# Performance work log

Measured on AMD Instinct MI355X. Metric: run time of the kernel, lower is better.

Reference implementation:

```python
import jax, jax.numpy as jnp
import numpy as np

D_MODEL = 1024
N_HEADS = 16
HEAD_DIM = D_MODEL // N_HEADS


def setup_inputs() -> dict:
    key = jax.random.key(0)
    ks = jax.random.split(key, 5)
    s_in = 1.0 / np.sqrt(D_MODEL)
    x = jax.random.normal(ks[0], (4, 2048, D_MODEL), dtype=jnp.float32)
    w_qkv = jax.random.uniform(ks[1], (3 * D_MODEL, D_MODEL), dtype=jnp.float32, minval=-s_in, maxval=s_in)
    b_qkv = jax.random.uniform(ks[2], (3 * D_MODEL,), dtype=jnp.float32, minval=-s_in, maxval=s_in)
    w_out = jax.random.uniform(ks[3], (D_MODEL, D_MODEL), dtype=jnp.float32, minval=-s_in, maxval=s_in)
    b_out = jax.random.uniform(ks[4], (D_MODEL,), dtype=jnp.float32, minval=-s_in, maxval=s_in)
    return {"x": x, "w_qkv": w_qkv, "b_qkv": b_qkv, "w_out": w_out, "b_out": b_out}


def reference(x, w_qkv, b_qkv, w_out, b_out):
    B, T, D = x.shape
    H, hd = N_HEADS, HEAD_DIM
    qkv = x @ w_qkv.T + b_qkv                      # [B, T, 3D]
    q, k, v = jnp.split(qkv, 3, axis=-1)
    # [B, H, T, hd]
    q = q.reshape(B, T, H, hd).transpose(0, 2, 1, 3)
    k = k.reshape(B, T, H, hd).transpose(0, 2, 1, 3)
    v = v.reshape(B, T, H, hd).transpose(0, 2, 1, 3)
    scale = 1.0 / np.sqrt(hd).astype(np.float32)
    attn = jnp.einsum('bhqd,bhkd->bhqk', q, k) * scale
    causal = jnp.triu(jnp.ones((T, T), dtype=bool), k=1)
    attn = jnp.where(causal, -jnp.inf, attn)
    attn = jax.nn.softmax(attn, axis=-1)
    out = jnp.einsum('bhqk,bhkd->bhqd', attn, v)
    out = out.transpose(0, 2, 1, 3).reshape(B, T, D)
    return out @ w_out.T + b_out
```

## Files before the change

### kernel.cpp

```cpp
#include <hip/hip_runtime.h>
#include <hip/hip_bf16.h>
#include <stdint.h>

#define D_MODEL 1024
#define NHEADS 16
#define HD 64
#define BB 4
#define TT 2048
#define MM (BB*TT)
#define NQKV (3*D_MODEL)
#define KK D_MODEL

typedef __attribute__((ext_vector_type(4))) float f32x4;
typedef __attribute__((ext_vector_type(8))) short bf16x8;

__device__ __forceinline__ unsigned short f2bf(float x){
    union { __hip_bfloat16 h; unsigned short u; } c;
    c.h = __float2bfloat16(x);
    return c.u;
}

__device__ __forceinline__ void gload_lds16(const void* g, void* l){
    __builtin_amdgcn_global_load_lds(
        (const __attribute__((address_space(1))) unsigned int*)g,
        (__attribute__((address_space(3))) unsigned int*)l,
        16, 0, 0);
}

__global__ void cast_kernel(const float* __restrict__ in,
                            unsigned short* __restrict__ out, int n4){
    int i = blockIdx.x * blockDim.x + threadIdx.x;
    if (i >= n4) return;
    float4 v = reinterpret_cast<const float4*>(in)[i];
    ushort4 o;
    o.x = f2bf(v.x); o.y = f2bf(v.y); o.z = f2bf(v.z); o.w = f2bf(v.w);
    reinterpret_cast<ushort4*>(out)[i] = o;
}

__global__ __launch_bounds__(256) void gemm_qkv(
    const unsigned short* __restrict__ A, const unsigned short* __restrict__ Bw,
    const float* __restrict__ bias,
    unsigned short* __restrict__ qb, unsigned short* __restrict__ kb,
    unsigned short* __restrict__ vtb)
{
    __shared__ alignas(16) unsigned short As[128*32];
    __shared__ alignas(16) unsigned short Bs[128*32];
    const int tiles_n = NQKV/128;
    int bm = (blockIdx.x / tiles_n) * 128;
    int bn = (blockIdx.x % tiles_n) * 128;
    int tid = threadIdx.x;
    int w = tid >> 6, l = tid & 63;
    int wr = (w >> 1) * 64, wc = (w & 1) * 64;
    int lr = l & 15, hi = l >> 4;

    f32x4 acc[4][4] = {};

    int srow = tid >> 2;
    int scol = (tid & 3) * 8;
    const unsigned short* Ap = A + (size_t)(bm + srow) * KK + scol;
    const unsigned short* Bp = Bw + (size_t)(bn + srow) * KK + scol;
    char* AsB = (char*)As + w * 1024;
    char* BsB = (char*)Bs + w * 1024;

    for (int k0 = 0; k0 < KK; k0 += 32) {
        __syncthreads();
        gload_lds16(Ap + k0,           AsB);
        gload_lds16(Ap + 64*KK + k0,   AsB + 4096);
        gload_lds16(Bp + k0,           BsB);
        gload_lds16(Bp + 64*KK + k0,   BsB + 4096);
        __syncthreads();
        bf16x8 af[4], bfr[4];
        #pragma unroll
        for (int m = 0; m < 4; m++)
            af[m] = *reinterpret_cast<const bf16x8*>(&As[(wr + m*16 + lr)*32 + hi*8]);
        #pragma unroll
        for (int n = 0; n < 4; n++)
            bfr[n] = *reinterpret_cast<const bf16x8*>(&Bs[(wc + n*16 + lr)*32 + hi*8]);
        #pragma unroll
        for (int m = 0; m < 4; m++)
            #pragma unroll
            for (int n = 0; n < 4; n++)
                acc[m][n] = __builtin_amdgcn_mfma_f32_16x16x32_bf16(af[m], bfr[n], acc[m][n], 0, 0, 0);
    }

    #pragma unroll
    for (int m = 0; m < 4; m++) {
        int gm = bm + wr + m*16 + hi*4;
        int b  = gm >> 11;
        int t  = gm & 2047;
        #pragma unroll
        for (int n = 0; n < 4; n++) {
            int gn = bn + wc + n*16 + lr;
            float bv = bias[gn];
            int sec = gn >> 10;
            int nn  = gn & 1023;
            int h = nn >> 6, d = nn & 63;
            int bh = b * NHEADS + h;
            if (sec == 2) {
                ushort4 pk;
                pk.x = f2bf(acc[m][n][0] + bv);
                pk.y = f2bf(acc[m][n][1] + bv);
                pk.z = f2bf(acc[m][n][2] + bv);
                pk.w = f2bf(acc[m][n][3] + bv);
                *reinterpret_cast<ushort4*>(&vtb[((size_t)bh*HD + d)*TT + t]) = pk;
            } else {
                unsigned short* dst = (sec == 0) ? qb : kb;
                #pragma unroll
                for (int r = 0; r < 4; r++)
                    dst[((size_t)bh*TT + t + r)*HD + d] = f2bf(acc[m][n][r] + bv);
            }
        }
    }
}

__global__ __launch_bounds__(512) void attn_kernel(
    const unsigned short* __restrict__ qb, const unsigned short* __restrict__ kb,
    const unsigned short* __restrict__ vtb, unsigned short* __restrict__ ao)
{
    __shared__ alignas(16) unsigned short Kb[2][64*64];
    __shared__ alignas(16) unsigned short Vb[2][64*64];
    __shared__ alignas(16) unsigned short Pl[8][16*64];

    const int bh = blockIdx.x;
    const int qt = (gridDim.y - 1) - blockIdx.y;
    const int tid = threadIdx.x;
    const int w = tid >> 6, l = tid & 63;
    const int lr = l & 15, hi = l >> 4;

    const int qbase = qt * 128;
    const int qrow  = qbase + w*16;
    const int ktmax = 2*qt + 1;

    const unsigned short* Qp = qb + ((size_t)bh*TT + qrow) * HD;
    bf16x8 qf0 = *reinterpret_cast<const bf16x8*>(Qp + lr*HD + hi*8);
    bf16x8 qf1 = *reinterpret_cast<const bf16x8*>(Qp + lr*HD + 32 + hi*8);

    const unsigned short* Kg = kb  + (size_t)bh*TT*HD;
    const unsigned short* Vg = vtb + (size_t)bh*HD*TT;

    const int srow = w*8 + (l >> 3);
    const int sc16 = (l & 7) ^ (srow & 7);
    char* KbL[2] = { (char*)&Kb[0][0] + w*1024, (char*)&Kb[1][0] + w*1024 };
    char* VbL[2] = { (char*)&Vb[0][0] + w*1024, (char*)&Vb[1][0] + w*1024 };

    gload_lds16(Kg + (size_t)srow*HD + sc16*8, KbL[0]);
    gload_lds16(Vg + (size_t)srow*TT + sc16*8, VbL[0]);
    __syncthreads();

    float mS = -3e38f, lS = 0.f;
    f32x4 o[4] = {};
    const float sc = 0.125f * 1.4426950408889634f;
    const int qg = qrow + lr;
    const int swp = (lr & 7) << 4;
    char* Pw = (char*)&Pl[w][0];

    int cur = 0;
    for (int kt = 0; kt <= ktmax; ++kt) {
        const int kbase = kt*64;
        if (kt < ktmax) {
            int knext = kbase + 64;
            gload_lds16(Kg + (size_t)(knext + srow)*HD + sc16*8, KbL[cur^1]);
            gload_lds16(Vg + (size_t)srow*TT + knext + sc16*8,   VbL[cur^1]);
        }
        if (kbase <= qrow + 15) {
            const char* Kl = (const char*)&Kb[cur][0];
            const char* Vl = (const char*)&Vb[cur][0];
            f32x4 s[4] = {};
            #pragma unroll
            for (int n = 0; n < 4; n++) {
                int rb = (n*16 + lr) * 128;
                bf16x8 kf0 = *reinterpret_cast<const bf16x8*>(Kl + rb + (( 0 + hi*16) ^ swp));
                bf16x8 kf1 = *reinterpret_cast<const bf16x8*>(Kl + rb + ((64 + hi*16) ^ swp));
                s[n] = __builtin_amdgcn_mfma_f32_16x16x32_bf16(kf0, qf0, s[n], 0, 0, 0);
                s[n] = __builtin_amdgcn_mfma_f32_16x16x32_bf16(kf1, qf1, s[n], 0, 0, 0);
            }
            if (kbase + 63 > qrow) {
                #pragma unroll
                for (int n = 0; n < 4; n++)
                    #pragma unroll
                    for (int r = 0; r < 4; r++)
                        if (kbase + n*16 + hi*4 + r > qg) s[n][r] = -3e38f;
            }
            float rm = s[0][0];
            #pragma unroll
            for (int n = 0; n < 4; n++)
                #pragma unroll
                for (int r = 0; r < 4; r++) rm = fmaxf(rm, s[n][r]);
            rm = fmaxf(rm, __shfl_xor(rm, 16, 64));
            rm = fmaxf(rm, __shfl_xor(rm, 32, 64));
            float newm = fmaxf(mS, rm);
            float al = exp2f(sc * (mS - newm));
            mS = newm;
            const float c0 = sc * newm;
            float rs = 0.f;
            #pragma unroll
            for (int n = 0; n < 4; n++) {
                float p0 = exp2f(fmaf(s[n][0], sc, -c0));
                float p1 = exp2f(fmaf(s[n][1], sc, -c0));
                float p2 = exp2f(fmaf(s[n][2], sc, -c0));
                float p3 = exp2f(fmaf(s[n][3], sc, -c0));
                rs += (p0 + p1) + (p2 + p3);
                ushort4 u;
                u.x = f2bf(p0); u.y = f2bf(p1); u.z = f2bf(p2); u.w = f2bf(p3);
                *reinterpret_cast<ushort4*>(Pw + (lr*128 + ((n*32 + hi*8) ^ swp))) = u;
            }
            rs += __shfl_xor(rs, 16, 64);
            rs += __shfl_xor(rs, 32, 64);
            lS = lS * al + rs;
            #pragma unroll
            for (int r = 0; r < 4; r++) {
                float alr = __shfl(al, hi*4 + r, 64);
                o[0][r] *= alr; o[1][r] *= alr; o[2][r] *= alr; o[3][r] *= alr;
            }
            bf16x8 pa0 = *reinterpret_cast<const bf16x8*>(Pw + (lr*128 + (( 0 + hi*16) ^ swp)));
            bf16x8 pa1 = *reinterpret_cast<const bf16x8*>(Pw + (lr*128 + ((64 + hi*16) ^ swp)));
            #pragma unroll
            for (int nd = 0; nd < 4; nd++) {
                int rb = (nd*16 + lr) * 128;
                bf16x8 vf0 = *reinterpret_cast<const bf16x8*>(Vl + rb + (( 0 + hi*16) ^ swp));
                bf16x8 vf1 = *reinterpret_cast<const bf16x8*>(Vl + rb + ((64 + hi*16) ^ swp));
                o[nd] = __builtin_amdgcn_mfma_f32_16x16x32_bf16(pa0, vf0, o[nd], 0, 0, 0);
                o[nd] = __builtin_amdgcn_mfma_f32_16x16x32_bf16(pa1, vf1, o[nd], 0, 0, 0);
            }
        }
        __syncthreads();
        cur ^= 1;
    }

    float inv = 1.0f / lS;
    int b = bh >> 4, h = bh & 15;
    #pragma unroll
    for (int r = 0; r < 4; r++) {
        float invr = __shfl(inv, hi*4 + r, 64);
        int t = qrow + hi*4 + r;
        #pragma unroll
        for (int nd = 0; nd < 4; nd++) {
            float val = o[nd][r] * invr;
            ao[((size_t)b*TT + t)*D_MODEL + h*HD + nd*16 + lr] = f2bf(val);
        }
    }
}

__global__ __launch_bounds__(256) void gemm_out(
    const unsigned short* __restrict__ A, const unsigned short* __restrict__ Bw,
    const float* __restrict__ bias, float* __restrict__ out)
{
    __shared__ alignas(16) unsigned short As[128*32];
    __shared__ alignas(16) unsigned short Bs[128*32];
    const int tiles_n = D_MODEL/128;
    int bm = (blockIdx.x / tiles_n) * 128;
    int bn = (blockIdx.x % tiles_n) * 128;
    int tid = threadIdx.x;
    int w = tid >> 6, l = tid & 63;
    int wr = (w >> 1) * 64, wc = (w & 1) * 64;
    int lr = l & 15, hi = l >> 4;

    f32x4 acc[4][4] = {};

    int srow = tid >> 2;
    int scol = (tid & 3) * 8;
    const unsigned short* Ap = A + (size_t)(bm + srow) * KK + scol;
    const unsigned short* Bp = Bw + (size_t)(bn + srow) * KK + scol;
    char* AsB = (char*)As + w * 1024;
    char* BsB = (char*)Bs + w * 1024;

    for (int k0 = 0; k0 < KK; k0 += 32) {
        __syncthreads();
        gload_lds16(Ap + k0,          AsB);
        gload_lds16(Ap + 64*KK + k0,  AsB + 4096);
        gload_lds16(Bp + k0,          BsB);
        gload_lds16(Bp + 64*KK + k0,  BsB + 4096);
        __syncthreads();
        bf16x8 af[4], bfr[4];
        #pragma unroll
        for (int m = 0; m < 4; m++)
            af[m] = *reinterpret_cast<const bf16x8*>(&As[(wr + m*16 + lr)*32 + hi*8]);
        #pragma unroll
        for (int n = 0; n < 4; n++)
            bfr[n] = *reinterpret_cast<const bf16x8*>(&Bs[(wc + n*16 + lr)*32 + hi*8]);
        #pragma unroll
        for (int m = 0; m < 4; m++)
            #pragma unroll
            for (int n = 0; n < 4; n++)
                acc[m][n] = __builtin_amdgcn_mfma_f32_16x16x32_bf16(af[m], bfr[n], acc[m][n], 0, 0, 0);
    }

    #pragma unroll
    for (int m = 0; m < 4; m++) {
        int gm = bm + wr + m*16 + hi*4;
        #pragma unroll
        for (int n = 0; n < 4; n++) {
            int gn = bn + wc + n*16 + lr;
            float bv = bias[gn];
            #pragma unroll
            for (int r = 0; r < 4; r++)
                out[(size_t)(gm + r)*D_MODEL + gn] = acc[m][n][r] + bv;
        }
    }
}

extern "C" void kernel_launch(void* const* d_in, const int* in_sizes, int n_in,
                              void* d_out, int out_size, void* d_ws, size_t ws_size,
                              hipStream_t stream) {
    const float* x     = (const float*)d_in[0];
    const float* w_qkv = (const float*)d_in[1];
    const float* b_qkv = (const float*)d_in[2];
    const float* w_out = (const float*)d_in[3];
    const float* b_out = (const float*)d_in[4];
    float* out = (float*)d_out;

    char* ws = (char*)d_ws;
    unsigned short* xbf   = (unsigned short*)(ws);
    unsigned short* wqkvb = (unsigned short*)(ws + (size_t)16777216);
    unsigned short* woutb = (unsigned short*)(ws + (size_t)23068672);
    unsigned short* qb    = (unsigned short*)(ws + (size_t)25165824);
    unsigned short* kb    = (unsigned short*)(ws + (size_t)41943040);
    unsigned short* vtb   = (unsigned short*)(ws + (size_t)58720256);
    unsigned short* aob   = xbf;

    cast_kernel<<<(MM*KK/4)/256,       256, 0, stream>>>(x,     xbf,   MM*KK/4);
    cast_kernel<<<(NQKV*KK/4)/256,     256, 0, stream>>>(w_qkv, wqkvb, NQKV*KK/4);
    cast_kernel<<<(D_MODEL*D_MODEL/4)/256, 256, 0, stream>>>(w_out, woutb, D_MODEL*D_MODEL/4);

    gemm_qkv<<<(MM/128)*(NQKV/128), 256, 0, stream>>>(xbf, wqkvb, b_qkv, qb, kb, vtb);
    attn_kernel<<<dim3(BB*NHEADS, TT/128), 512, 0, stream>>>(qb, kb, vtb, aob);
    gemm_out<<<(MM/128)*(D_MODEL/128), 256, 0, stream>>>(aob, woutb, b_out, out);
}
```

Before: 184.1 us.

## Double-buffer GEMM tiles, remap workgroups, lazy softmax rescale, fuse casts

Both GEMMs now double-buffer their LDS tiles, so the next K slice is fetched while MFMAs run on the current one, leaving one barrier per iteration instead of two. Workgroup IDs are remapped across 8 groups to change how tiles are spread over the chiplets and caches. The attention kernel skips the online-softmax rescale of the output accumulator unless the running max grows past a threshold, and raises wave priority around its MFMA sections. The three cast launches are merged into one kernel. Doubled LDS use may lower occupancy, and the lazy rescale lets the exponentials grow up to 2^8 before renormalising.

Result: faster. 179.9 us (-2.3%).

```diff
diff --git a/kernel.cpp b/kernel.cpp
--- a/kernel.cpp
+++ b/kernel.cpp
@@ -27,14 +27,22 @@
         16, 0, 0);
 }
 
-__global__ void cast_kernel(const float* __restrict__ in,
-                            unsigned short* __restrict__ out, int n4){
+#define N4_X  (MM*KK/4)
+#define N4_WQ (NQKV*KK/4)
+#define N4_WO (D_MODEL*D_MODEL/4)
+__global__ void cast3_kernel(const float* __restrict__ x, const float* __restrict__ wq,
+                             const float* __restrict__ wo,
+                             unsigned short* __restrict__ xb, unsigned short* __restrict__ wqb,
+                             unsigned short* __restrict__ wob){
     int i = blockIdx.x * blockDim.x + threadIdx.x;
-    if (i >= n4) return;
-    float4 v = reinterpret_cast<const float4*>(in)[i];
+    const float* src; unsigned short* dst; int j;
+    if (i < N4_X)              { src = x;  dst = xb;  j = i; }
+    else if (i < N4_X + N4_WQ) { src = wq; dst = wqb; j = i - N4_X; }
+    else                       { src = wo; dst = wob; j = i - N4_X - N4_WQ; }
+    float4 v = reinterpret_cast<const float4*>(src)[j];
     ushort4 o;
     o.x = f2bf(v.x); o.y = f2bf(v.y); o.z = f2bf(v.z); o.w = f2bf(v.w);
-    reinterpret_cast<ushort4*>(out)[i] = o;
+    reinterpret_cast<ushort4*>(dst)[j] = o;
 }
 
 __global__ __launch_bounds__(256) void gemm_qkv(
@@ -43,11 +51,14 @@
     unsigned short* __restrict__ qb, unsigned short* __restrict__ kb,
     unsigned short* __restrict__ vtb)
 {
-    __shared__ alignas(16) unsigned short As[128*32];
-    __shared__ alignas(16) unsigned short Bs[128*32];
+    __shared__ alignas(16) unsigned short As[2][128*32];
+    __shared__ alignas(16) unsigned short Bs[2][128*32];
     const int tiles_n = NQKV/128;
-    int bm = (blockIdx.x / tiles_n) * 128;
-    int bn = (blockIdx.x % tiles_n) * 128;
+    int nwg = gridDim.x;
+    int orig = blockIdx.x;
+    int bid = (orig & 7) * (nwg >> 3) + (orig >> 3);
+    int bm = (bid / tiles_n) * 128;
+    int bn = (bid % tiles_n) * 128;
     int tid = threadIdx.x;
     int w = tid >> 6, l = tid & 63;
     int wr = (w >> 1) * 64, wc = (w & 1) * 64;
@@ -59,28 +70,43 @@
     int scol = (tid & 3) * 8;
     const unsigned short* Ap = A + (size_t)(bm + srow) * KK + scol;
     const unsigned short* Bp = Bw + (size_t)(bn + srow) * KK + scol;
-    char* AsB = (char*)As + w * 1024;
-    char* BsB = (char*)Bs + w * 1024;
-
+
+    {
+        char* AsB = (char*)&As[0][0] + w*1024;
+        char* BsB = (char*)&Bs[0][0] + w*1024;
+        gload_lds16(Ap,           AsB);
+        gload_lds16(Ap + 64*KK,   AsB + 4096);
+        gload_lds16(Bp,           BsB);
+        gload_lds16(Bp + 64*KK,   BsB + 4096);
+    }
+    __syncthreads();
+
+    int cur = 0;
     for (int k0 = 0; k0 < KK; k0 += 32) {
-        __syncthreads();
-        gload_lds16(Ap + k0,           AsB);
-        gload_lds16(Ap + 64*KK + k0,   AsB + 4096);
-        gload_lds16(Bp + k0,           BsB);
-        gload_lds16(Bp + 64*KK + k0,   BsB + 4096);
-        __syncthreads();
+        if (k0 + 32 < KK) {
+            char* AsB = (cur ? (char*)&As[0][0] : (char*)&As[1][0]) + w*1024;
+            char* BsB = (cur ? (char*)&Bs[0][0] : (char*)&Bs[1][0]) + w*1024;
+            gload_lds16(Ap + k0 + 32,          AsB);
+            gload_lds16(Ap + 64*KK + k0 + 32,  AsB + 4096);
+            gload_lds16(Bp + k0 + 32,          BsB);
+            gload_lds16(Bp + 64*KK + k0 + 32,  BsB + 4096);
+        }
+        const unsigned short* Ab = cur ? &As[1][0] : &As[0][0];
+        const unsigned short* Bb = cur ? &Bs[1][0] : &Bs[0][0];
         bf16x8 af[4], bfr[4];
         #pragma unroll
         for (int m = 0; m < 4; m++)
-            af[m] = *reinterpret_cast<const bf16x8*>(&As[(wr + m*16 + lr)*32 + hi*8]);
+            af[m] = *reinterpret_cast<const bf16x8*>(&Ab[(wr + m*16 + lr)*32 + hi*8]);
         #pragma unroll
         for (int n = 0; n < 4; n++)
-            bfr[n] = *reinterpret_cast<const bf16x8*>(&Bs[(wc + n*16 + lr)*32 + hi*8]);
+            bfr[n] = *reinterpret_cast<const bf16x8*>(&Bb[(wc + n*16 + lr)*32 + hi*8]);
         #pragma unroll
         for (int m = 0; m < 4; m++)
             #pragma unroll
             for (int n = 0; n < 4; n++)
                 acc[m][n] = __builtin_amdgcn_mfma_f32_16x16x32_bf16(af[m], bfr[n], acc[m][n], 0, 0, 0);
+        __syncthreads();
+        cur ^= 1;
     }
 
     #pragma unroll
@@ -140,16 +166,19 @@
 
     const int srow = w*8 + (l >> 3);
     const int sc16 = (l & 7) ^ (srow & 7);
-    char* KbL[2] = { (char*)&Kb[0][0] + w*1024, (char*)&Kb[1][0] + w*1024 };
-    char* VbL[2] = { (char*)&Vb[0][0] + w*1024, (char*)&Vb[1][0] + w*1024 };
-
-    gload_lds16(Kg + (size_t)srow*HD + sc16*8, KbL[0]);
-    gload_lds16(Vg + (size_t)srow*TT + sc16*8, VbL[0]);
+    char* KbL0 = (char*)&Kb[0][0] + w*1024;
+    char* KbL1 = (char*)&Kb[1][0] + w*1024;
+    char* VbL0 = (char*)&Vb[0][0] + w*1024;
+    char* VbL1 = (char*)&Vb[1][0] + w*1024;
+
+    gload_lds16(Kg + (size_t)srow*HD + sc16*8, KbL0);
+    gload_lds16(Vg + (size_t)srow*TT + sc16*8, VbL0);
     __syncthreads();
 
     float mS = -3e38f, lS = 0.f;
     f32x4 o[4] = {};
     const float sc = 0.125f * 1.4426950408889634f;
+    const float THR = 8.0f / sc;
     const int qg = qrow + lr;
     const int swp = (lr & 7) << 4;
     char* Pw = (char*)&Pl[w][0];
@@ -159,13 +188,16 @@
         const int kbase = kt*64;
         if (kt < ktmax) {
             int knext = kbase + 64;
-            gload_lds16(Kg + (size_t)(knext + srow)*HD + sc16*8, KbL[cur^1]);
-            gload_lds16(Vg + (size_t)srow*TT + knext + sc16*8,   VbL[cur^1]);
+            char* kd = cur ? KbL0 : KbL1;
+            char* vd = cur ? VbL0 : VbL1;
+            gload_lds16(Kg + (size_t)(knext + srow)*HD + sc16*8, kd);
+            gload_lds16(Vg + (size_t)srow*TT + knext + sc16*8,   vd);
         }
         if (kbase <= qrow + 15) {
-            const char* Kl = (const char*)&Kb[cur][0];
-            const char* Vl = (const char*)&Vb[cur][0];
+            const char* Kl = cur ? (const char*)&Kb[1][0] : (const char*)&Kb[0][0];
+            const char* Vl = cur ? (const char*)&Vb[1][0] : (const char*)&Vb[0][0];
             f32x4 s[4] = {};
+            __builtin_amdgcn_s_setprio(1);
             #pragma unroll
             for (int n = 0; n < 4; n++) {
                 int rb = (n*16 + lr) * 128;
@@ -174,6 +206,7 @@
                 s[n] = __builtin_amdgcn_mfma_f32_16x16x32_bf16(kf0, qf0, s[n], 0, 0, 0);
                 s[n] = __builtin_amdgcn_mfma_f32_16x16x32_bf16(kf1, qf1, s[n], 0, 0, 0);
             }
+            __builtin_amdgcn_s_setprio(0);
             if (kbase + 63 > qrow) {
                 #pragma unroll
                 for (int n = 0; n < 4; n++)
@@ -181,17 +214,25 @@
                     for (int r = 0; r < 4; r++)
                         if (kbase + n*16 + hi*4 + r > qg) s[n][r] = -3e38f;
             }
-            float rm = s[0][0];
-            #pragma unroll
-            for (int n = 0; n < 4; n++)
-                #pragma unroll
-                for (int r = 0; r < 4; r++) rm = fmaxf(rm, s[n][r]);
+            float t0 = fmaxf(fmaxf(s[0][0], s[0][1]), fmaxf(s[0][2], s[0][3]));
+            float t1 = fmaxf(fmaxf(s[1][0], s[1][1]), fmaxf(s[1][2], s[1][3]));
+            float t2 = fmaxf(fmaxf(s[2][0], s[2][1]), fmaxf(s[2][2], s[2][3]));
+            float t3 = fmaxf(fmaxf(s[3][0], s[3][1]), fmaxf(s[3][2], s[3][3]));
+            float rm = fmaxf(fmaxf(t0, t1), fmaxf(t2, t3));
             rm = fmaxf(rm, __shfl_xor(rm, 16, 64));
             rm = fmaxf(rm, __shfl_xor(rm, 32, 64));
-            float newm = fmaxf(mS, rm);
-            float al = exp2f(sc * (mS - newm));
-            mS = newm;
-            const float c0 = sc * newm;
+            if (!__all(rm - mS <= THR)) {
+                float newm = fmaxf(mS, rm);
+                float al = exp2f(sc * (mS - newm));
+                mS = newm;
+                lS *= al;
+                #pragma unroll
+                for (int r = 0; r < 4; r++) {
+                    float alr = __shfl(al, hi*4 + r, 64);
+                    o[0][r] *= alr; o[1][r] *= alr; o[2][r] *= alr; o[3][r] *= alr;
+                }
+            }
+            const float c0 = sc * mS;
             float rs = 0.f;
             #pragma unroll
             for (int n = 0; n < 4; n++) {
@@ -206,14 +247,10 @@
             }
             rs += __shfl_xor(rs, 16, 64);
             rs += __shfl_xor(rs, 32, 64);
-            lS = lS * al + rs;
-            #pragma unroll
-            for (int r = 0; r < 4; r++) {
-                float alr = __shfl(al, hi*4 + r, 64);
-                o[0][r] *= alr; o[1][r] *= alr; o[2][r] *= alr; o[3][r] *= alr;
-            }
+            lS += rs;
             bf16x8 pa0 = *reinterpret_cast<const bf16x8*>(Pw + (lr*128 + (( 0 + hi*16) ^ swp)));
             bf16x8 pa1 = *reinterpret_cast<const bf16x8*>(Pw + (lr*128 + ((64 + hi*16) ^ swp)));
+            __builtin_amdgcn_s_setprio(1);
             #pragma unroll
             for (int nd = 0; nd < 4; nd++) {
                 int rb = (nd*16 + lr) * 128;
@@ -222,6 +259,7 @@
                 o[nd] = __builtin_amdgcn_mfma_f32_16x16x32_bf16(pa0, vf0, o[nd], 0, 0, 0);
                 o[nd] = __builtin_amdgcn_mfma_f32_16x16x32_bf16(pa1, vf1, o[nd], 0, 0, 0);
             }
+            __builtin_amdgcn_s_setprio(0);
         }
         __syncthreads();
         cur ^= 1;
@@ -245,11 +283,14 @@
     const unsigned short* __restrict__ A, const unsigned short* __restrict__ Bw,
     const float* __restrict__ bias, float* __restrict__ out)
 {
-    __shared__ alignas(16) unsigned short As[128*32];
-    __shared__ alignas(16) unsigned short Bs[128*32];
+    __shared__ alignas(16) unsigned short As[2][128*32];
+    __shared__ alignas(16) unsigned short Bs[2][128*32];
     const int tiles_n = D_MODEL/128;
-    int bm = (blockIdx.x / tiles_n) * 128;
-    int bn = (blockIdx.x % tiles_n) * 128;
+    int nwg = gridDim.x;
+    int orig = blockIdx.x;
+    int bid = (orig & 7) * (nwg >> 3) + (orig >> 3);
+    int bm = (bid / tiles_n) * 128;
+    int bn = (bid % tiles_n) * 128;
     int tid = threadIdx.x;
     int w = tid >> 6, l = tid & 63;
     int wr = (w >> 1) * 64, wc = (w & 1) * 64;
@@ -261,28 +302,43 @@
     int scol = (tid & 3) * 8;
     const unsigned short* Ap = A + (size_t)(bm + srow) * KK + scol;
     const unsigned short* Bp = Bw + (size_t)(bn + srow) * KK + scol;
-    char* AsB = (char*)As + w * 1024;
-    char* BsB = (char*)Bs + w * 1024;
-
+
+    {
+        char* AsB = (char*)&As[0][0] + w*1024;
+        char* BsB = (char*)&Bs[0][0] + w*1024;
+        gload_lds16(Ap,           AsB);
+        gload_lds16(Ap + 64*KK,   AsB + 4096);
+        gload_lds16(Bp,           BsB);
+        gload_lds16(Bp + 64*KK,   BsB + 4096);
+    }
+    __syncthreads();
+
+    int cur = 0;
     for (int k0 = 0; k0 < KK; k0 += 32) {
-        __syncthreads();
-        gload_lds16(Ap + k0,          AsB);
-        gload_lds16(Ap + 64*KK + k0,  AsB + 4096);
-        gload_lds16(Bp + k0,          BsB);
-        gload_lds16(Bp + 64*KK + k0,  BsB + 4096);
-        __syncthreads();
+        if (k0 + 32 < KK) {
+            char* AsB = (cur ? (char*)&As[0][0] : (char*)&As[1][0]) + w*1024;
+            char* BsB = (cur ? (char*)&Bs[0][0] : (char*)&Bs[1][0]) + w*1024;
+            gload_lds16(Ap + k0 + 32,          AsB);
+            gload_lds16(Ap + 64*KK + k0 + 32,  AsB + 4096);
+            gload_lds16(Bp + k0 + 32,          BsB);
+            gload_lds16(Bp + 64*KK + k0 + 32,  BsB + 4096);
+        }
+        const unsigned short* Ab = cur ? &As[1][0] : &As[0][0];
+        const unsigned short* Bb = cur ? &Bs[1][0] : &Bs[0][0];
         bf16x8 af[4], bfr[4];
         #pragma unroll
         for (int m = 0; m < 4; m++)
-            af[m] = *reinterpret_cast<const bf16x8*>(&As[(wr + m*16 + lr)*32 + hi*8]);
+            af[m] = *reinterpret_cast<const bf16x8*>(&Ab[(wr + m*16 + lr)*32 + hi*8]);
         #pragma unroll
         for (int n = 0; n < 4; n++)
-            bfr[n] = *reinterpret_cast<const bf16x8*>(&Bs[(wc + n*16 + lr)*32 + hi*8]);
+            bfr[n] = *reinterpret_cast<const bf16x8*>(&Bb[(wc + n*16 + lr)*32 + hi*8]);
         #pragma unroll
         for (int m = 0; m < 4; m++)
             #pragma unroll
             for (int n = 0; n < 4; n++)
                 acc[m][n] = __builtin_amdgcn_mfma_f32_16x16x32_bf16(af[m], bfr[n], acc[m][n], 0, 0, 0);
+        __syncthreads();
+        cur ^= 1;
     }
 
     #pragma unroll
@@ -318,9 +374,7 @@
     unsigned short* vtb   = (unsigned short*)(ws + (size_t)58720256);
     unsigned short* aob   = xbf;
 
-    cast_kernel<<<(MM*KK/4)/256,       256, 0, stream>>>(x,     xbf,   MM*KK/4);
-    cast_kernel<<<(NQKV*KK/4)/256,     256, 0, stream>>>(w_qkv, wqkvb, NQKV*KK/4);
-    cast_kernel<<<(D_MODEL*D_MODEL/4)/256, 256, 0, stream>>>(w_out, woutb, D_MODEL*D_MODEL/4);
+    cast3_kernel<<<(N4_X + N4_WQ + N4_WO)/256, 256, 0, stream>>>(x, w_qkv, w_out, xbf, wqkvb, woutb);
 
     gemm_qkv<<<(MM/128)*(NQKV/128), 256, 0, stream>>>(xbf, wqkvb, b_qkv, qb, kb, vtb);
     attn_kernel<<<dim3(BB*NHEADS, TT/128), 512, 0, stream>>>(qb, kb, vtb, aob);
```
